# Kernel optimization log

Hardware: AMD Instinct MI355X
Metric: run time of the kernel (lower is better)

## Reference

```python
import jax, jax.numpy as jnp
import numpy as np

N, E = 50000, 500000
IN_C, HID, OUT_C, HEADS, NL = 128, 16, 16, 8, 4
EPS = 1e-5
NEG_SLOPE = 0.2


def _gatv2(x, src, dst, Wl, Wr, att, bias, concat):
    # GATv2Conv (PyG semantics, eval mode): lin_l on source, lin_r on target,
    # e = a . LeakyReLU(xl[src] + xr[dst]); segment softmax over dst; scatter-sum.
    n = x.shape[0]
    H, C = att.shape
    xl = (x @ Wl).reshape(n, H, C)
    xr = (x @ Wr).reshape(n, H, C)
    e = jax.nn.leaky_relu(xl[src] + xr[dst], NEG_SLOPE)          # [E', H, C]
    logit = jnp.einsum('ehc,hc->eh', e, att)                      # [E', H]
    mx = jax.lax.stop_gradient(jax.ops.segment_max(logit, dst, num_segments=n))
    a = jnp.exp(logit - mx[dst])
    denom = jax.ops.segment_sum(a, dst, num_segments=n)
    alpha = a / denom[dst]                                        # [E', H]
    out = jax.ops.segment_sum(xl[src] * alpha[..., None], dst, num_segments=n)
    out = out.reshape(n, H * C) if concat else out.mean(axis=1)
    return out + bias


def _bn_eval(x, g, b, m, v):
    return (x - m) * jax.lax.rsqrt(v + EPS) * g + b


def setup_inputs() -> dict:
    key = jax.random.key(0)
    ks = jax.random.split(key, 32)
    d = {}
    d['x'] = jax.random.normal(ks[0], (N, IN_C), dtype=jnp.float32)
    d['edge_index'] = jax.random.randint(ks[1], (2, E), 0, N, dtype=jnp.int64)
    HC = HID * HEADS  # 128
    dims_in = [IN_C, HC, HC, HC]
    dims_h = [HEADS, HEADS, HEADS, 1]
    dims_c = [HID, HID, HID, OUT_C]
    ki = 2
    for i in range(NL):
        fan = dims_in[i]
        s = 1.0 / np.sqrt(fan)
        d[f'W{i}l'] = jax.random.uniform(ks[ki], (fan, dims_h[i] * dims_c[i]), minval=-s, maxval=s, dtype=jnp.float32); ki += 1
        d[f'W{i}r'] = jax.random.uniform(ks[ki], (fan, dims_h[i] * dims_c[i]), minval=-s, maxval=s, dtype=jnp.float32); ki += 1
        d[f'a{i}'] = jax.random.normal(ks[ki], (dims_h[i], dims_c[i]), dtype=jnp.float32) * 0.1; ki += 1
        out_dim = dims_h[i] * dims_c[i] if i < NL - 1 else dims_c[i]
        d[f'b{i}'] = jnp.zeros((out_dim,), dtype=jnp.float32)
    for i in range(NL - 1):
        d[f'g{i}'] = jnp.ones((HC,), dtype=jnp.float32) + 0.1 * jax.random.normal(ks[ki], (HC,), dtype=jnp.float32); ki += 1
        d[f'be{i}'] = 0.1 * jax.random.normal(ks[ki], (HC,), dtype=jnp.float32); ki += 1
        d[f'm{i}'] = 0.1 * jax.random.normal(ks[ki], (HC,), dtype=jnp.float32); ki += 1
        d[f'v{i}'] = jnp.ones((HC,), dtype=jnp.float32)
    return d


def reference(x, edge_index, W0l, W0r, a0, b0, W1l, W1r, a1, b1, W2l, W2r, a2, b2, W3l, W3r, a3, b3, g0, be0, m0, v0, g1, be1, m1, v1, g2, be2, m2, v2):
    n = x.shape[0]
    loop = jnp.arange(n, dtype=edge_index.dtype)
    src = jnp.concatenate([edge_index[0], loop])  # add_self_loops=True (PyG default)
    dst = jnp.concatenate([edge_index[1], loop])
    Ws = [(W0l, W0r, a0, b0), (W1l, W1r, a1, b1), (W2l, W2r, a2, b2), (W3l, W3r, a3, b3)]
    bns = [(g0, be0, m0, v0), (g1, be1, m1, v1), (g2, be2, m2, v2)]
    h = x
    for i in range(NL):
        Wl, Wr, att, bias = Ws[i]
        h = _gatv2(h, src, dst, Wl, Wr, att, bias, concat=(i < NL - 1))
        if i < NL - 1:
            g, b, m, v = bns[i]
            h = jax.nn.elu(_bn_eval(h, g, b, m, v))
    return h
```

## Files before the change

kernel.cpp:

```cpp
#include <hip/hip_runtime.h>
#include <hip/hip_fp16.h>
#include <math.h>

static constexpr float BN_EPS = 1e-5f;
static constexpr float NEG = 0.2f;

typedef float f32x4 __attribute__((ext_vector_type(4)));
typedef _Float16 h16x2 __attribute__((ext_vector_type(2)));
typedef _Float16 h16x8 __attribute__((ext_vector_type(8)));


__global__ __launch_bounds__(256) void hist_pack(
    const int* __restrict__ ei, int E, int n, int* __restrict__ cnt,
    const float* __restrict__ W0l, const float* __restrict__ W0r,
    const float* __restrict__ W1l, const float* __restrict__ W1r,
    const float* __restrict__ W2l, const float* __restrict__ W2r,
    const float* __restrict__ W3l, const float* __restrict__ W3r,
    __half* __restrict__ pk0, __half* __restrict__ pk1,
    __half* __restrict__ pk2, __half* __restrict__ pk3,
    const float* __restrict__ b0, const float* __restrict__ b1,
    const float* __restrict__ b2,
    const float* __restrict__ g0, const float* __restrict__ g1,
    const float* __restrict__ g2,
    const float* __restrict__ be0, const float* __restrict__ be1,
    const float* __restrict__ be2,
    const float* __restrict__ m0, const float* __restrict__ m1,
    const float* __restrict__ m2,
    const float* __restrict__ v0, const float* __restrict__ v1,
    const float* __restrict__ v2,
    float* __restrict__ bnA, float* __restrict__ bnB) {
    int b = blockIdx.x;
    if (b < 200) {
        if (threadIdx.x >= 64) return;
        const float *Wl, *Wr;
        __half* packed;
        int tile, NTT, M;
        if (b < 192) {
            int layer = b >> 6;
            tile = b & 63;
            NTT = 16; M = 128;
            Wl = (layer == 0) ? W0l : (layer == 1) ? W1l : W2l;
            Wr = (layer == 0) ? W0r : (layer == 1) ? W1r : W2r;
            packed = (layer == 0) ? pk0 : (layer == 1) ? pk1 : pk2;
        } else {
            tile = b - 192;
            NTT = 2; M = 16;
            Wl = W3l; Wr = W3r; packed = pk3;
        }
        int NT = NTT >> 1;
        int gnt = tile % NTT;
        int kt = tile / NTT;
        int l = threadIdx.x;
        const float* W = (gnt < NT) ? Wl : Wr;
        int col = (gnt % NT) * 16 + (l & 15);
        int krow = kt * 32 + ((l >> 4) << 3);
        size_t base = (size_t)tile * 512 + (size_t)l * 8;
#pragma unroll
        for (int j = 0; j < 8; j++)
            packed[base + j] = __float2half(W[(size_t)(krow + j) * M + col]);
    } else if (b == 200) {
        for (int t = threadIdx.x; t < 384; t += 256) {
            int layer = t >> 7;
            int c = t & 127;
            const float* gg = (layer == 0) ? g0 : (layer == 1) ? g1 : g2;
            const float* ee = (layer == 0) ? be0 : (layer == 1) ? be1 : be2;
            const float* mm = (layer == 0) ? m0 : (layer == 1) ? m1 : m2;
            const float* vv = (layer == 0) ? v0 : (layer == 1) ? v1 : v2;
            const float* bb = (layer == 0) ? b0 : (layer == 1) ? b1 : b2;
            float A = gg[c] * rsqrtf(vv[c] + BN_EPS);
            bnA[t] = A;
            bnB[t] = fmaf(bb[c] - mm[c], A, ee[c]);
        }
    } else {
        int e = (b - 201) * 256 + threadIdx.x;
        int ET = E + n;
        if (e >= ET) return;
        int d = (e < E) ? ei[E + e] : (e - E);
        atomicAdd(&cnt[d], 1);
    }
}


__device__ __forceinline__ void scan_block_body256(
    const int* __restrict__ cnt, int* __restrict__ rowptr,
    int* __restrict__ bsums, int n, int bid, int* s) {
    int t = threadIdx.x;
    int base = bid * 1024 + t * 4;
    int v0 = 0, v1 = 0, v2 = 0, v3 = 0;
    if (base + 3 < n) {
        v0 = cnt[base];     v1 = cnt[base + 1];
        v2 = cnt[base + 2]; v3 = cnt[base + 3];
    } else {
        if (base < n)     v0 = cnt[base];
        if (base + 1 < n) v1 = cnt[base + 1];
        if (base + 2 < n) v2 = cnt[base + 2];
        if (base + 3 < n) v3 = cnt[base + 3];
    }
    int p1 = v0 + v1, p2 = p1 + v2, p3 = p2 + v3;
    s[t] = p3;
    __syncthreads();
    for (int d = 1; d < 256; d <<= 1) {
        int tt = (t >= d) ? s[t - d] : 0;
        __syncthreads();
        s[t] += tt;
        __syncthreads();
    }
    int ex = s[t] - p3;
    if (base < n)     rowptr[base + 1] = ex + v0;
    if (base + 1 < n) rowptr[base + 2] = ex + p1;
    if (base + 2 < n) rowptr[base + 3] = ex + p2;
    if (base + 3 < n) rowptr[base + 4] = ex + p3;
    if (t == 255) bsums[bid] = s[255];
}

__global__ __launch_bounds__(256) void scan_only(
    const int* __restrict__ cnt, int* __restrict__ rowraw,
    int* __restrict__ bsums, int n) {
    __shared__ int s[256];
    scan_block_body256(cnt, rowraw, bsums, n, blockIdx.x, s);
}


template <bool FIRST>
__device__ __forceinline__ void gemm_body(
    const __half* __restrict__ xh, const float* __restrict__ xf,
    const __half* __restrict__ packed,
    __half* __restrict__ Y1, __half* __restrict__ Y2, int n, int bid,
    _Float16* sA) {
    const int t = threadIdx.x;
    const int row0 = bid * 64;

    for (int c = t; c < 1024; c += 256) {
        int row = c >> 4;
        int off = (c & 15) * 8;
        int gr = row0 + row;
        if (gr >= n) gr = n - 1;
        if (FIRST) {
            float4 v0 = *(const float4*)&xf[(size_t)gr * 128 + off];
            float4 v1 = *(const float4*)&xf[(size_t)gr * 128 + off + 4];
            h16x8 h = {(_Float16)v0.x, (_Float16)v0.y, (_Float16)v0.z, (_Float16)v0.w,
                       (_Float16)v1.x, (_Float16)v1.y, (_Float16)v1.z, (_Float16)v1.w};
            *(h16x8*)&sA[row * 136 + off] = h;
        } else {
            *(h16x8*)&sA[row * 136 + off] = *(const h16x8*)&xh[(size_t)gr * 128 + off];
        }
    }
    __syncthreads();

    const int lane = t & 63;
    const int s = t >> 6;
    const int lr = lane & 15;
    const int kq = (lane >> 4) * 8;

    h16x8 af[4][4];
#pragma unroll
    for (int rt = 0; rt < 4; rt++)
#pragma unroll
        for (int kt = 0; kt < 4; kt++)
            af[rt][kt] = *(const h16x8*)&sA[(rt * 16 + lr) * 136 + kt * 32 + kq];

    f32x4 acc[4][4];
#pragma unroll
    for (int a = 0; a < 4; a++)
#pragma unroll
        for (int b = 0; b < 4; b++) acc[a][b] = (f32x4){0.f, 0.f, 0.f, 0.f};

#pragma unroll
    for (int kt = 0; kt < 4; kt++) {
#pragma unroll
        for (int ntl = 0; ntl < 4; ntl++) {
            int nt = s * 4 + ntl;
            h16x8 b = *(const h16x8*)&packed[((size_t)(kt * 16 + nt)) * 512 + lane * 8];
#pragma unroll
            for (int rt = 0; rt < 4; rt++)
                acc[ntl][rt] = __builtin_amdgcn_mfma_f32_16x16x32_f16(af[rt][kt], b, acc[ntl][rt], 0, 0, 0);
        }
    }

    __half* Y = (s < 2) ? Y1 : Y2;
    const int colh = (s & 1) * 64;
    const int rq = (lane >> 4) * 4;
#pragma unroll
    for (int ntl = 0; ntl < 4; ntl++) {
        int col = colh + ntl * 16 + lr;
#pragma unroll
        for (int rt = 0; rt < 4; rt++) {
#pragma unroll
            for (int g = 0; g < 4; g++) {
                int row = row0 + rt * 16 + rq + g;
                if (row < n) Y[(size_t)row * 128 + col] = __float2half(acc[ntl][rt][g]);
            }
        }
    }
}

__global__ __launch_bounds__(256) void gemm_h_big2(
    const __half* __restrict__ xh, const __half* __restrict__ packed,
    __half* __restrict__ Y1, __half* __restrict__ Y2, int n) {
    __shared__ __align__(16) char smem[64 * 136 * 2];
    gemm_body<false>(xh, nullptr, packed, Y1, Y2, n, blockIdx.x, (_Float16*)smem);
}


__global__ __launch_bounds__(256) void scatfin_gemm0(
    const int* __restrict__ ei, int E, int n,
    const int* __restrict__ rowraw, const int* __restrict__ bsums, int nb,
    int* __restrict__ fill, int* __restrict__ col, int* __restrict__ rowfin,
    const float* __restrict__ xf, const __half* __restrict__ packed,
    __half* __restrict__ Y1, __half* __restrict__ Y2, int gb, int nbF) {
    __shared__ __align__(16) char smem[64 * 136 * 2];
    int b = blockIdx.x;
    if (b < gb) {
        gemm_body<true>(nullptr, xf, packed, Y1, Y2, n, b, (_Float16*)smem);
        return;
    }
    int* spre = (int*)smem;
    if (threadIdx.x < 64) {
        int L = threadIdx.x;
        int bv = (L < nb) ? bsums[L] : 0;
#pragma unroll
        for (int d = 1; d < 64; d <<= 1) {
            int t = __shfl_up(bv, d);
            if (L >= d) bv += t;
        }
        int ex = __shfl_up(bv, 1);
        if (L == 0) ex = 0;
        spre[L] = ex;
    }
    __syncthreads();
    b -= gb;
    if (b < nbF) {
        int i0 = b * 1024 + threadIdx.x * 4;
#pragma unroll
        for (int j = 0; j < 4; j++) {
            int i = i0 + j;
            if (i < n) rowfin[i + 1] = rowraw[i + 1] + spre[i >> 10];
        }
        if (b == 0 && threadIdx.x == 0) rowfin[0] = 0;
    } else {
        int e = (b - nbF) * 256 + threadIdx.x;
        int ET = E + n;
        if (e >= ET) return;
        int s, d;
        if (e < E) { s = ei[e]; d = ei[E + e]; } else { s = e - E; d = s; }
        int pos = atomicAdd(&fill[d], 1);
        int base = (d == 0) ? 0 : (rowraw[d] + spre[(d - 1) >> 10]);
        col[base + pos] = s;
    }
}


__global__ __launch_bounds__(256) void gemm_h_small(
    const __half* __restrict__ xh, const __half* __restrict__ packed,
    float* __restrict__ Y1, float* __restrict__ Y2, int n) {
    int lane = threadIdx.x & 63;
    int wv = blockIdx.x * 4 + (threadIdx.x >> 6);
    int row0 = wv * 16;
    if (row0 >= n) return;
    int r = row0 + (lane & 15);
    if (r >= n) r = n - 1;
    int kq = (lane >> 4) * 8;

    h16x8 af[4];
#pragma unroll
    for (int kt = 0; kt < 4; kt++)
        af[kt] = *(const h16x8*)&xh[(size_t)r * 128 + kt * 32 + kq];

    f32x4 acc[2];
    acc[0] = (f32x4){0.f, 0.f, 0.f, 0.f};
    acc[1] = (f32x4){0.f, 0.f, 0.f, 0.f};

#pragma unroll
    for (int kt = 0; kt < 4; kt++) {
#pragma unroll
        for (int nt = 0; nt < 2; nt++) {
            h16x8 b = *(const h16x8*)&packed[((size_t)(kt * 2 + nt)) * 512 + lane * 8];
            acc[nt] = __builtin_amdgcn_mfma_f32_16x16x32_f16(af[kt], b, acc[nt], 0, 0, 0);
        }
    }

    int colb = lane & 15;
    int rbase = row0 + (lane >> 4) * 4;
#pragma unroll
    for (int nt = 0; nt < 2; nt++) {
        float* Y = (nt == 0) ? Y1 : Y2;
#pragma unroll
        for (int g = 0; g < 4; g++) {
            int row = rbase + g;
            if (row < n) Y[(size_t)row * 16 + colb] = acc[nt][g];
        }
    }
}


__global__ __launch_bounds__(256) void agg_h(
    const __half* __restrict__ xl, const __half* __restrict__ xr,
    const int* __restrict__ rowptr, const int* __restrict__ col,
    const float* __restrict__ att,
    const float* __restrict__ bnA, const float* __restrict__ bnB,
    __half* __restrict__ oh, int n) {
    int v = (blockIdx.x * blockDim.x + threadIdx.x) >> 3;
    if (v >= n) return;
    int L = threadIdx.x & 7;
    int ch = L * 16;

    int beg = rowptr[v];
    int end = rowptr[v + 1];
    int cb = beg;
    int cidx = (cb + L < end) ? col[cb + L] : v;

    const __half* xrb = &xr[((size_t)v << 7) + ch];
    h16x8 rx0 = *(const h16x8*)xrb;
    h16x8 rx1 = *(const h16x8*)(xrb + 8);
    float4 af0 = *(const float4*)&att[ch];
    float4 af1 = *(const float4*)&att[ch + 4];
    float4 af2 = *(const float4*)&att[ch + 8];
    float4 af3 = *(const float4*)&att[ch + 12];
    h16x2 a[8] = {{(_Float16)af0.x, (_Float16)af0.y}, {(_Float16)af0.z, (_Float16)af0.w},
                  {(_Float16)af1.x, (_Float16)af1.y}, {(_Float16)af1.z, (_Float16)af1.w},
                  {(_Float16)af2.x, (_Float16)af2.y}, {(_Float16)af2.z, (_Float16)af2.w},
                  {(_Float16)af3.x, (_Float16)af3.y}, {(_Float16)af3.z, (_Float16)af3.w}};
    const h16x8 neg8 = {(_Float16)NEG, (_Float16)NEG, (_Float16)NEG, (_Float16)NEG,
                        (_Float16)NEG, (_Float16)NEG, (_Float16)NEG, (_Float16)NEG};

    float lrun = 0.f;
    float acc[16];
#pragma unroll
    for (int k = 0; k < 16; k++) acc[k] = 0.f;

    while (true) {
        int nxtb = cb + 8;
        bool more = (nxtb < end);
        int cidx_n = v;
        if (more && (nxtb + L < end)) cidx_n = col[nxtb + L];
        int ce = min(end, nxtb);
        for (int e = cb; e < ce; e += 4) {
            int off = e - cb;
            h16x8 hv0[4], hv1[4];
#pragma unroll
            for (int j = 0; j < 4; j++) {
                int u = __shfl(cidx, off + j, 8);
                const __half* s = &xl[((size_t)u << 7) + ch];
                hv0[j] = *(const h16x8*)s;
                hv1[j] = *(const h16x8*)(s + 8);
            }
#pragma unroll
            for (int j = 0; j < 4; j++) {
                bool ok = (e + j < end);
                h16x8 s0 = hv0[j] + rx0;
                h16x8 s1 = hv1[j] + rx1;
                h16x8 l0 = __builtin_elementwise_max(s0, s0 * neg8);
                h16x8 l1 = __builtin_elementwise_max(s1, s1 * neg8);
                const h16x2* l0p = (const h16x2*)&l0;
                const h16x2* l1p = (const h16x2*)&l1;
#if __has_builtin(__builtin_amdgcn_fdot2)
                float part = __builtin_amdgcn_fdot2(l0p[0], a[0], 0.f, false);
                part = __builtin_amdgcn_fdot2(l0p[1], a[1], part, false);
                part = __builtin_amdgcn_fdot2(l0p[2], a[2], part, false);
                part = __builtin_amdgcn_fdot2(l0p[3], a[3], part, false);
                part = __builtin_amdgcn_fdot2(l1p[0], a[4], part, false);
                part = __builtin_amdgcn_fdot2(l1p[1], a[5], part, false);
                part = __builtin_amdgcn_fdot2(l1p[2], a[6], part, false);
                part = __builtin_amdgcn_fdot2(l1p[3], a[7], part, false);
#else
                float part = 0.f;
#pragma unroll
                for (int i = 0; i < 4; i++)
                    part += (float)l0p[i].x * (float)a[i].x + (float)l0p[i].y * (float)a[i].y
                          + (float)l1p[i].x * (float)a[4 + i].x + (float)l1p[i].y * (float)a[4 + i].y;
#endif
                float p = ok ? __expf(part) : 0.f;
                lrun += p;
                const _Float16* h0 = (const _Float16*)&hv0[j];
                const _Float16* h1 = (const _Float16*)&hv1[j];
#pragma unroll
                for (int k = 0; k < 8; k++) acc[k] = fmaf(p, (float)h0[k], acc[k]);
#pragma unroll
                for (int k = 0; k < 8; k++) acc[8 + k] = fmaf(p, (float)h1[k], acc[8 + k]);
            }
        }
        if (!more) break;
        cb = nxtb;
        cidx = cidx_n;
    }

    float inv = 1.0f / lrun;
    float4 A0 = *(const float4*)&bnA[ch];
    float4 A1 = *(const float4*)&bnA[ch + 4];
    float4 A2 = *(const float4*)&bnA[ch + 8];
    float4 A3 = *(const float4*)&bnA[ch + 12];
    float4 B0 = *(const float4*)&bnB[ch];
    float4 B1 = *(const float4*)&bnB[ch + 4];
    float4 B2 = *(const float4*)&bnB[ch + 8];
    float4 B3 = *(const float4*)&bnB[ch + 12];
    float Av[16] = {A0.x, A0.y, A0.z, A0.w, A1.x, A1.y, A1.z, A1.w,
                    A2.x, A2.y, A2.z, A2.w, A3.x, A3.y, A3.z, A3.w};
    float Bv[16] = {B0.x, B0.y, B0.z, B0.w, B1.x, B1.y, B1.z, B1.w,
                    B2.x, B2.y, B2.z, B2.w, B3.x, B3.y, B3.z, B3.w};
    h16x8 o0, o1;
#pragma unroll
    for (int k = 0; k < 8; k++) {
        float o = fmaf(acc[k], inv * Av[k], Bv[k]);
        o = o > 0.f ? o : expm1f(o);
        o0[k] = (_Float16)o;
    }
#pragma unroll
    for (int k = 0; k < 8; k++) {
        float o = fmaf(acc[8 + k], inv * Av[8 + k], Bv[8 + k]);
        o = o > 0.f ? o : expm1f(o);
        o1[k] = (_Float16)o;
    }
    __half* ob = &oh[((size_t)v << 7) + ch];
    *(h16x8*)ob = o0;
    *(h16x8*)(ob + 8) = o1;
}


__global__ __launch_bounds__(256) void agg_f(
    const float* __restrict__ xl, const float* __restrict__ xr,
    const int* __restrict__ rowptr, const int* __restrict__ col,
    const float* __restrict__ att, const float* __restrict__ bias,
    float* __restrict__ out, int n) {
    int v = (blockIdx.x * blockDim.x + threadIdx.x) >> 2;
    if (v >= n) return;
    int L = threadIdx.x & 3;
    int ch = 4 * L;

    int beg = rowptr[v];
    int end = rowptr[v + 1];
    int cb = beg;
    int cidx = (cb + L < end) ? col[cb + L] : v;

    float4 xrv = *(const float4*)&xr[((size_t)v << 4) + ch];
    float4 av = *(const float4*)&att[ch];

    float lrun = 0.f;
    float4 acc = make_float4(0.f, 0.f, 0.f, 0.f);

    while (true) {
        float4 xv[4];
#pragma unroll
        for (int j = 0; j < 4; j++) {
            int u = __shfl(cidx, j, 4);
            xv[j] = *(const float4*)&xl[((size_t)u << 4) + ch];
        }
#pragma unroll
        for (int j = 0; j < 4; j++) {
            bool ok = (cb + j < end);
            float s0 = xv[j].x + xrv.x; s0 = s0 > 0.f ? s0 : NEG * s0;
            float s1 = xv[j].y + xrv.y; s1 = s1 > 0.f ? s1 : NEG * s1;
            float s2 = xv[j].z + xrv.z; s2 = s2 > 0.f ? s2 : NEG * s2;
            float s3 = xv[j].w + xrv.w; s3 = s3 > 0.f ? s3 : NEG * s3;
            float part = fmaf(s0, av.x, fmaf(s1, av.y, fmaf(s2, av.z, s3 * av.w)));
            part += __shfl_xor(part, 1);
            part += __shfl_xor(part, 2);
            float p = ok ? __expf(part) : 0.f;
            lrun += p;
            acc.x = fmaf(p, xv[j].x, acc.x);
            acc.y = fmaf(p, xv[j].y, acc.y);
            acc.z = fmaf(p, xv[j].z, acc.z);
            acc.w = fmaf(p, xv[j].w, acc.w);
        }
        cb += 4;
        if (cb >= end) break;
        cidx = (cb + L < end) ? col[cb + L] : v;
    }

    float inv = 1.0f / lrun;
    float4 b4 = *(const float4*)&bias[ch];
    *(float4*)&out[((size_t)v << 4) + ch] =
        make_float4(fmaf(acc.x, inv, b4.x), fmaf(acc.y, inv, b4.y),
                    fmaf(acc.z, inv, b4.z), fmaf(acc.w, inv, b4.w));
}


extern "C" void kernel_launch(void* const* d_in, const int* in_sizes, int n_in,
                              void* d_out, int out_size, void* d_ws, size_t ws_size,
                              hipStream_t stream) {
    const float* x = (const float*)d_in[0];
    const int* ei = (const int*)d_in[1];
    const float* Wl[4] = {(const float*)d_in[2], (const float*)d_in[6],
                          (const float*)d_in[10], (const float*)d_in[14]};
    const float* Wr[4] = {(const float*)d_in[3], (const float*)d_in[7],
                          (const float*)d_in[11], (const float*)d_in[15]};
    const float* att[4] = {(const float*)d_in[4], (const float*)d_in[8],
                           (const float*)d_in[12], (const float*)d_in[16]};
    const float* bias[4] = {(const float*)d_in[5], (const float*)d_in[9],
                            (const float*)d_in[13], (const float*)d_in[17]};
    const float* g[3] = {(const float*)d_in[18], (const float*)d_in[22], (const float*)d_in[26]};
    const float* be[3] = {(const float*)d_in[19], (const float*)d_in[23], (const float*)d_in[27]};
    const float* bm[3] = {(const float*)d_in[20], (const float*)d_in[24], (const float*)d_in[28]};
    const float* bv[3] = {(const float*)d_in[21], (const float*)d_in[25], (const float*)d_in[29]};

    const int n = in_sizes[0] / 128;
    const int E = in_sizes[1] / 2;
    const int ET = E + n;

    char* p = (char*)d_ws;
    __half* xh = (__half*)p;           p += (size_t)n * 128 * 2;
    __half* xlh = (__half*)p;          p += (size_t)n * 128 * 2;
    __half* xrh = (__half*)p;          p += (size_t)n * 128 * 2;
    float* xl3 = (float*)p;            p += (size_t)n * 16 * 4;
    float* xr3 = (float*)p;            p += (size_t)n * 16 * 4;
    int* rowraw = (int*)p;            p += (size_t)(n + 4) * 4;
    int* rowfin = (int*)p;            p += (size_t)(n + 4) * 4;
    int* cnt = (int*)p;               p += (size_t)n * 4;
    int* fill = (int*)p;              p += (size_t)n * 4;
    int* col = (int*)p;               p += (size_t)ET * 4;
    int* bsums = (int*)p;             p += 256;
    __half* pk[4];
    for (int i = 0; i < 3; i++) { pk[i] = (__half*)p; p += 4 * 16 * 512 * 2; }
    pk[3] = (__half*)p;               p += 4 * 2 * 512 * 2;
    float* bnA = (float*)p;           p += 384 * 4;
    float* bnB = (float*)p;           p += 384 * 4;

    (void)hipMemsetAsync(cnt, 0, (size_t)n * 8, stream);

    const int tb = 256;
    const int histBlocks = (ET + tb - 1) / tb;
    hist_pack<<<201 + histBlocks, tb, 0, stream>>>(
        ei, E, n, cnt,
        Wl[0], Wr[0], Wl[1], Wr[1], Wl[2], Wr[2], Wl[3], Wr[3],
        pk[0], pk[1], pk[2], pk[3],
        bias[0], bias[1], bias[2],
        g[0], g[1], g[2], be[0], be[1], be[2],
        bm[0], bm[1], bm[2], bv[0], bv[1], bv[2],
        bnA, bnB);

    const int nb = (n + 1023) / 1024;
    const int gb64 = (n + 63) / 64;
    const int gemmBlocksSmall = ((n + 15) / 16 + 3) / 4;
    const int aggBlocksH = (n + 31) / 32;
    const int aggBlocksF = (n + 63) / 64;

    scan_only<<<nb, 256, 0, stream>>>(cnt, rowraw, bsums, n);

    scatfin_gemm0<<<gb64 + nb + histBlocks, 256, 0, stream>>>(
        ei, E, n, rowraw, bsums, nb, fill, col, rowfin,
        x, pk[0], xlh, xrh, gb64, nb);

    agg_h<<<aggBlocksH, 256, 0, stream>>>(
        xlh, xrh, rowfin, col, att[0], bnA, bnB, xh, n);
    for (int i = 1; i < 3; i++) {
        gemm_h_big2<<<gb64, 256, 0, stream>>>(xh, pk[i], xlh, xrh, n);
        agg_h<<<aggBlocksH, 256, 0, stream>>>(
            xlh, xrh, rowfin, col, att[i], bnA + 128 * i, bnB + 128 * i, xh, n);
    }
    gemm_h_small<<<gemmBlocksSmall, 256, 0, stream>>>(xh, pk[3], xl3, xr3, n);
    agg_f<<<aggBlocksF, 256, 0, stream>>>(
        xl3, xr3, rowfin, col, att[3], bias[3], (float*)d_out, n);
}
```

Baseline: 336.8 us.

## Restructure CSR build pipeline and vectorize GEMM output stores via swapped MFMA operands

Moves the per-block scan into the first GEMM launch and splits the prefix fix-up and edge scatter into separate kernels, so the row pointer array is finalized in place. The scatter then reads a single finished offset per edge instead of recomputing it. It also swaps the MFMA A/B operands so each lane holds consecutive output columns, which lets the GEMM kernels write vectorized ushort4/float4 stores instead of scalar ones. The kernel count goes up by one, and the edge scatter can no longer overlap with the layer-0 GEMM.

```diff
diff --git a/kernel.cpp b/kernel.cpp
--- a/kernel.cpp
+++ b/kernel.cpp
@@ -113,11 +113,37 @@
     if (t == 255) bsums[bid] = s[255];
 }
 
-__global__ __launch_bounds__(256) void scan_only(
-    const int* __restrict__ cnt, int* __restrict__ rowraw,
-    int* __restrict__ bsums, int n) {
-    __shared__ int s[256];
-    scan_block_body256(cnt, rowraw, bsums, n, blockIdx.x, s);
+__global__ __launch_bounds__(1024) void scan_add2(
+    int* __restrict__ rowptr, const int* __restrict__ bsums, int n, int nb) {
+    __shared__ int sex;
+    if (threadIdx.x < 64) {
+        int L = threadIdx.x;
+        int v = (L < nb) ? bsums[L] : 0;
+#pragma unroll
+        for (int d = 1; d < 64; d <<= 1) {
+            int t = __shfl_up(v, d);
+            if (L >= d) v += t;
+        }
+        int ex = __shfl_up(v, 1);
+        if (L == 0) ex = 0;
+        if (L == (int)blockIdx.x) sex = ex;
+    }
+    __syncthreads();
+    int i = blockIdx.x * 1024 + threadIdx.x;
+    if (i < n) rowptr[i + 1] += sex;
+    if (i == 0) rowptr[0] = 0;
+}
+
+__global__ void scatter_kernel(const int* __restrict__ ei, int E, int n,
+                               const int* __restrict__ rowptr, int* __restrict__ fill,
+                               int* __restrict__ col) {
+    int e = blockIdx.x * blockDim.x + threadIdx.x;
+    int ET = E + n;
+    if (e >= ET) return;
+    int s, d;
+    if (e < E) { s = ei[e]; d = ei[E + e]; } else { s = e - E; d = s; }
+    int pos = atomicAdd(&fill[d], 1);
+    col[rowptr[d] + pos] = s;
 }
 
 
@@ -173,7 +199,7 @@
             h16x8 b = *(const h16x8*)&packed[((size_t)(kt * 16 + nt)) * 512 + lane * 8];
 #pragma unroll
             for (int rt = 0; rt < 4; rt++)
-                acc[ntl][rt] = __builtin_amdgcn_mfma_f32_16x16x32_f16(af[rt][kt], b, acc[ntl][rt], 0, 0, 0);
+                acc[ntl][rt] = __builtin_amdgcn_mfma_f32_16x16x32_f16(b, af[rt][kt], acc[ntl][rt], 0, 0, 0);
         }
     }
 
@@ -181,15 +207,18 @@
     const int colh = (s & 1) * 64;
     const int rq = (lane >> 4) * 4;
 #pragma unroll
-    for (int ntl = 0; ntl < 4; ntl++) {
-        int col = colh + ntl * 16 + lr;
-#pragma unroll
-        for (int rt = 0; rt < 4; rt++) {
-#pragma unroll
-            for (int g = 0; g < 4; g++) {
-                int row = row0 + rt * 16 + rq + g;
-                if (row < n) Y[(size_t)row * 128 + col] = __float2half(acc[ntl][rt][g]);
-            }
+    for (int rt = 0; rt < 4; rt++) {
+        int row = row0 + rt * 16 + lr;
+        if (row >= n) continue;
+#pragma unroll
+        for (int ntl = 0; ntl < 4; ntl++) {
+            int c0 = colh + ntl * 16 + rq;
+            ushort4 o = make_ushort4(
+                __half_as_ushort(__float2half(acc[ntl][rt][0])),
+                __half_as_ushort(__float2half(acc[ntl][rt][1])),
+                __half_as_ushort(__float2half(acc[ntl][rt][2])),
+                __half_as_ushort(__float2half(acc[ntl][rt][3])));
+            *(ushort4*)&Y[(size_t)row * 128 + c0] = o;
         }
     }
 }
@@ -201,51 +230,18 @@
     gemm_body<false>(xh, nullptr, packed, Y1, Y2, n, blockIdx.x, (_Float16*)smem);
 }
 
-
-__global__ __launch_bounds__(256) void scatfin_gemm0(
-    const int* __restrict__ ei, int E, int n,
-    const int* __restrict__ rowraw, const int* __restrict__ bsums, int nb,
-    int* __restrict__ fill, int* __restrict__ col, int* __restrict__ rowfin,
+__global__ __launch_bounds__(256) void scanblk_gemm0(
+    const int* __restrict__ cnt, int* __restrict__ rowptr,
+    int* __restrict__ bsums, int n, int nscan,
     const float* __restrict__ xf, const __half* __restrict__ packed,
-    __half* __restrict__ Y1, __half* __restrict__ Y2, int gb, int nbF) {
+    __half* __restrict__ Y1, __half* __restrict__ Y2) {
     __shared__ __align__(16) char smem[64 * 136 * 2];
     int b = blockIdx.x;
-    if (b < gb) {
-        gemm_body<true>(nullptr, xf, packed, Y1, Y2, n, b, (_Float16*)smem);
-        return;
-    }
-    int* spre = (int*)smem;
-    if (threadIdx.x < 64) {
-        int L = threadIdx.x;
-        int bv = (L < nb) ? bsums[L] : 0;
-#pragma unroll
-        for (int d = 1; d < 64; d <<= 1) {
-            int t = __shfl_up(bv, d);
-            if (L >= d) bv += t;
-        }
-        int ex = __shfl_up(bv, 1);
-        if (L == 0) ex = 0;
-        spre[L] = ex;
-    }
-    __syncthreads();
-    b -= gb;
-    if (b < nbF) {
-        int i0 = b * 1024 + threadIdx.x * 4;
-#pragma unroll
-        for (int j = 0; j < 4; j++) {
-            int i = i0 + j;
-            if (i < n) rowfin[i + 1] = rowraw[i + 1] + spre[i >> 10];
-        }
-        if (b == 0 && threadIdx.x == 0) rowfin[0] = 0;
+    if (b < nscan) {
+        scan_block_body256(cnt, rowptr, bsums, n, b, (int*)smem);
     } else {
-        int e = (b - nbF) * 256 + threadIdx.x;
-        int ET = E + n;
-        if (e >= ET) return;
-        int s, d;
-        if (e < E) { s = ei[e]; d = ei[E + e]; } else { s = e - E; d = s; }
-        int pos = atomicAdd(&fill[d], 1);
-        int base = (d == 0) ? 0 : (rowraw[d] + spre[(d - 1) >> 10]);
-        col[base + pos] = s;
+        gemm_body<true>(nullptr, xf, packed, Y1, Y2, n, b - nscan,
+                        (_Float16*)smem);
     }
 }
 
@@ -258,13 +254,13 @@
     int row0 = wv * 16;
     if (row0 >= n) return;
     int r = row0 + (lane & 15);
-    if (r >= n) r = n - 1;
+    int rl = (r >= n) ? (n - 1) : r;
     int kq = (lane >> 4) * 8;
 
     h16x8 af[4];
 #pragma unroll
     for (int kt = 0; kt < 4; kt++)
-        af[kt] = *(const h16x8*)&xh[(size_t)r * 128 + kt * 32 + kq];
+        af[kt] = *(const h16x8*)&xh[(size_t)rl * 128 + kt * 32 + kq];
 
     f32x4 acc[2];
     acc[0] = (f32x4){0.f, 0.f, 0.f, 0.f};
@@ -275,19 +271,17 @@
 #pragma unroll
         for (int nt = 0; nt < 2; nt++) {
             h16x8 b = *(const h16x8*)&packed[((size_t)(kt * 2 + nt)) * 512 + lane * 8];
-            acc[nt] = __builtin_amdgcn_mfma_f32_16x16x32_f16(af[kt], b, acc[nt], 0, 0, 0);
-        }
-    }
-
-    int colb = lane & 15;
-    int rbase = row0 + (lane >> 4) * 4;
-#pragma unroll
-    for (int nt = 0; nt < 2; nt++) {
-        float* Y = (nt == 0) ? Y1 : Y2;
-#pragma unroll
-        for (int g = 0; g < 4; g++) {
-            int row = rbase + g;
-            if (row < n) Y[(size_t)row * 16 + colb] = acc[nt][g];
+            acc[nt] = __builtin_amdgcn_mfma_f32_16x16x32_f16(b, af[kt], acc[nt], 0, 0, 0);
+        }
+    }
+
+    if (r < n) {
+        int rq = (lane >> 4) * 4;
+#pragma unroll
+        for (int nt = 0; nt < 2; nt++) {
+            float* Y = (nt == 0) ? Y1 : Y2;
+            *(float4*)&Y[(size_t)r * 16 + rq] =
+                make_float4(acc[nt][0], acc[nt][1], acc[nt][2], acc[nt][3]);
         }
     }
 }
@@ -502,8 +496,7 @@
     __half* xrh = (__half*)p;          p += (size_t)n * 128 * 2;
     float* xl3 = (float*)p;            p += (size_t)n * 16 * 4;
     float* xr3 = (float*)p;            p += (size_t)n * 16 * 4;
-    int* rowraw = (int*)p;            p += (size_t)(n + 4) * 4;
-    int* rowfin = (int*)p;            p += (size_t)(n + 4) * 4;
+    int* rowptr = (int*)p;            p += (size_t)(n + 4) * 4;
     int* cnt = (int*)p;               p += (size_t)n * 4;
     int* fill = (int*)p;              p += (size_t)n * 4;
     int* col = (int*)p;               p += (size_t)ET * 4;
@@ -533,20 +526,19 @@
     const int aggBlocksH = (n + 31) / 32;
     const int aggBlocksF = (n + 63) / 64;
 
-    scan_only<<<nb, 256, 0, stream>>>(cnt, rowraw, bsums, n);
-
-    scatfin_gemm0<<<gb64 + nb + histBlocks, 256, 0, stream>>>(
-        ei, E, n, rowraw, bsums, nb, fill, col, rowfin,
-        x, pk[0], xlh, xrh, gb64, nb);
+    scanblk_gemm0<<<nb + gb64, 256, 0, stream>>>(
+        cnt, rowptr, bsums, n, nb, x, pk[0], xlh, xrh);
+    scan_add2<<<nb, 1024, 0, stream>>>(rowptr, bsums, n, nb);
+    scatter_kernel<<<(ET + tb - 1) / tb, tb, 0, stream>>>(ei, E, n, rowptr, fill, col);
 
     agg_h<<<aggBlocksH, 256, 0, stream>>>(
-        xlh, xrh, rowfin, col, att[0], bnA, bnB, xh, n);
+        xlh, xrh, rowptr, col, att[0], bnA, bnB, xh, n);
     for (int i = 1; i < 3; i++) {
         gemm_h_big2<<<gb64, 256, 0, stream>>>(xh, pk[i], xlh, xrh, n);
         agg_h<<<aggBlocksH, 256, 0, stream>>>(
-            xlh, xrh, rowfin, col, att[i], bnA + 128 * i, bnB + 128 * i, xh, n);
+            xlh, xrh, rowptr, col, att[i], bnA + 128 * i, bnB + 128 * i, xh, n);
     }
     gemm_h_small<<<gemmBlocksSmall, 256, 0, stream>>>(xh, pk[3], xl3, xr3, n);
     agg_f<<<aggBlocksF, 256, 0, stream>>>(
-        xl3, xr3, rowfin, col, att[3], bias[3], (float*)d_out, n);
-}
+        xl3, xr3, rowptr, col, att[3], bias[3], (float*)d_out, n);
+}
```

New measurement: 338.7 us. About the same (+0.6%).
